# Performance work log

Measured on AMD Instinct MI355X. Metric: run time of the kernel, lower is better.

Reference implementation:

```python
import jax, jax.numpy as jnp
import numpy as np

NUM_GRAPHS = 4096


def setup_inputs() -> dict:
    key = jax.random.key(0)
    k1, k2, k3, k4, k5 = jax.random.split(key, 5)
    N, H = 500000, 256
    x = jax.random.normal(k1, (N, H), dtype=jnp.float32)
    batch = jnp.sort(jax.random.randint(k2, (N,), 0, NUM_GRAPHS, dtype=jnp.int64))
    # gate MLP: Linear(H, H//2) -> tanh -> Linear(H//2, 1)
    W1 = jax.random.normal(k3, (H, H // 2), dtype=jnp.float32) / np.sqrt(H)
    b1 = jnp.zeros((H // 2,), dtype=jnp.float32)
    W2 = jax.random.normal(k4, (H // 2, 1), dtype=jnp.float32) / np.sqrt(H // 2)
    b2 = jnp.zeros((1,), dtype=jnp.float32)
    return {"x": x, "batch": batch, "W1": W1, "b1": b1, "W2": W2, "b2": b2}


def reference(x, batch, W1, b1, W2, b2):
    # gate scores per node: (N,)
    h = jnp.tanh(x @ W1 + b1)
    scores = (h @ W2 + b2).squeeze(-1)
    # segment (per-graph) softmax over nodes
    seg_max = jax.ops.segment_max(scores, batch, num_segments=NUM_GRAPHS)
    # empty segments give -inf max; guard so gather stays finite
    seg_max = jnp.where(jnp.isfinite(seg_max), seg_max, 0.0)
    ex = jnp.exp(scores - seg_max[batch])
    seg_sum = jax.ops.segment_sum(ex, batch, num_segments=NUM_GRAPHS)
    weights = ex / seg_sum[batch]  # (N,)
    # weighted scatter-add pooling -> (B, H)
    pooled = jax.ops.segment_sum(weights[:, None] * x, batch, num_segments=NUM_GRAPHS)
    return pooled, weights
```

## Files before the change

kernel.cpp:

```cpp
#include <hip/hip_runtime.h>
#include <hip/hip_bf16.h>

#define NGRAPH 4096

typedef __attribute__((ext_vector_type(8))) short s16x8;
typedef __attribute__((ext_vector_type(4))) float f32x4;
typedef unsigned int u32;

__device__ inline short f2bf(float f) {
  unsigned u = __float_as_uint(f);
  unsigned r = u + 0x7fffu + ((u >> 16) & 1u);
  return (short)(r >> 16);
}

__global__ void prepack_w1(const float* __restrict__ W1, s16x8* __restrict__ w1p) {
  int t = blockIdx.x * 256 + threadIdx.x;
  int f = t >> 6, l = t & 63;
  int kt = f >> 3, ct = f & 7;
  int k0 = kt * 32 + ((l >> 4) * 8);
  int c  = ct * 16 + (l & 15);
  s16x8 v;
  #pragma unroll
  for (int e = 0; e < 8; ++e) v[e] = f2bf(W1[(k0 + e) * 128 + c]);
  w1p[f * 64 + l] = v;
}

__device__ inline long long getb(const void* b, int i, int is64) {
  if (is64) return ((const long long*)b)[i];
  return (long long)((const int*)b)[i];
}

__device__ inline int lowb(const void* b, int n, long long v, int is64) {
  int lo = 0, hi = n;
  while (lo < hi) {
    int mid = (lo + hi) >> 1;
    if (getb(b, mid, is64) < v) lo = mid + 1; else hi = mid;
  }
  return lo;
}

__device__ inline int batch_is64(const void* batch, int N) {
  int probe = ((N & 1) == 0) ? (N - 1) : (N - 2);
  return (((const int*)batch)[probe] == 0) ? 1 : 0;
}

__global__ void seg_offsets(const void* __restrict__ batch, int* __restrict__ offs, int N) {
  int g = blockIdx.x * 256 + threadIdx.x;
  const int is64 = batch_is64(batch, N);
  if (g <= NGRAPH) offs[g] = lowb(batch, N, (long long)g, is64);
}

__device__ inline float fast_tanh(float v) {
  v = fminf(fmaxf(v, -15.f), 15.f);
  float e = __expf(2.f * v);
  return __fdividef(e - 1.f, e + 1.f);
}

__device__ inline void dma16(const float* src, char* ldsdst) {
  __builtin_amdgcn_global_load_lds(
      (const __attribute__((address_space(1))) u32*)src,
      (__attribute__((address_space(3))) u32*)ldsdst,
      16, 0, 0);
}

__global__ __launch_bounds__(256, 3)
void gate_pool(const float* __restrict__ x, const int* __restrict__ offs,
               const float* __restrict__ b1, const float* __restrict__ W2,
               const float* __restrict__ b2p, const s16x8* __restrict__ w1p,
               float* __restrict__ pooled, float* __restrict__ expout,
               float* __restrict__ segsum, int N)
{
  __shared__ __align__(16) char tile[32 * 1024];
  __shared__ float sp[2][32];
  __shared__ float sw[32];

  const int tid = threadIdx.x;
  const int w = tid >> 6, l = tid & 63;
  const int colhalf = w & 1, wp = w >> 1;
  const int l15 = l & 15, lg = l >> 4;
  const int node0 = blockIdx.x * 32;

  #pragma unroll
  for (int i = 0; i < 8; ++i) {
    const int r = i * 4 + w;
    int grow = node0 + r;
    if (grow >= N) grow = N - 1;
    const float* src = x + (size_t)grow * 256 + ((l ^ (r & 7)) << 2);
    dma16(src, tile + r * 1024);
  }

  float b1v[4], w2v[4];
  #pragma unroll
  for (int ct = 0; ct < 4; ++ct) {
    int c = colhalf * 64 + ct * 16 + l15;
    b1v[ct] = b1[c];
    w2v[ct] = W2[c];
  }
  const float b2s = b2p[0];

  __syncthreads();

  {
    const int r0 = wp * 16 + l15;
    const char* p0 = tile + r0 * 1024;
    const int s0 = (r0 & 7);

    f32x4 acc0 = {0.f,0.f,0.f,0.f}, acc1 = {0.f,0.f,0.f,0.f};
    f32x4 acc2 = {0.f,0.f,0.f,0.f}, acc3 = {0.f,0.f,0.f,0.f};
    #pragma unroll
    for (int kt = 0; kt < 8; ++kt) {
      const int cc = kt * 8 + lg * 2;
      float4 xa = *(const float4*)(p0 + (((cc    ) ^ s0) << 4));
      float4 xb = *(const float4*)(p0 + (((cc + 1) ^ s0) << 4));
      const s16x8* wb = w1p + (kt * 8 + colhalf * 4) * 64 + l;
      s16x8 bf0 = wb[0], bf1 = wb[64], bf2 = wb[128], bf3 = wb[192];
      s16x8 a;
      a[0] = f2bf(xa.x); a[1] = f2bf(xa.y); a[2] = f2bf(xa.z); a[3] = f2bf(xa.w);
      a[4] = f2bf(xb.x); a[5] = f2bf(xb.y); a[6] = f2bf(xb.z); a[7] = f2bf(xb.w);
      acc0 = __builtin_amdgcn_mfma_f32_16x16x32_bf16(a, bf0, acc0, 0, 0, 0);
      acc1 = __builtin_amdgcn_mfma_f32_16x16x32_bf16(a, bf1, acc1, 0, 0, 0);
      acc2 = __builtin_amdgcn_mfma_f32_16x16x32_bf16(a, bf2, acc2, 0, 0, 0);
      acc3 = __builtin_amdgcn_mfma_f32_16x16x32_bf16(a, bf3, acc3, 0, 0, 0);
    }
    float part[4];
    #pragma unroll
    for (int r = 0; r < 4; ++r) {
      part[r] = colhalf ? 0.f : b2s;
      part[r] += fast_tanh(acc0[r] + b1v[0]) * w2v[0];
      part[r] += fast_tanh(acc1[r] + b1v[1]) * w2v[1];
      part[r] += fast_tanh(acc2[r] + b1v[2]) * w2v[2];
      part[r] += fast_tanh(acc3[r] + b1v[3]) * w2v[3];
    }
    #pragma unroll
    for (int m = 1; m <= 8; m <<= 1) {
      #pragma unroll
      for (int r = 0; r < 4; ++r) part[r] += __shfl_xor(part[r], m, 64);
    }
    if (l15 == 0) {
      #pragma unroll
      for (int r = 0; r < 4; ++r)
        sp[colhalf][wp * 16 + lg * 4 + r] = part[r];
    }
  }
  __syncthreads();

  if (tid < 32) {
    int node = node0 + tid;
    float e = 0.f;
    if (node < N) {
      e = __expf(sp[0][tid] + sp[1][tid]);
      expout[node] = e;
    }
    sw[tid] = e;
  }
  __syncthreads();

  const int nmax = min(32, N - node0);
  int g;
  {
    int lo = 0, hi = NGRAPH - 1;
    while (lo < hi) {
      int mid = (lo + hi) >> 1;
      if (offs[mid + 1] <= node0) lo = mid + 1; else hi = mid;
    }
    g = lo;
  }
  const int ccb = tid >> 2, cib = (tid & 3) << 2;
  int r = 0;
  int nb = offs[g + 1];
  while (r < nmax) {
    const int rend = min(nb - node0, nmax);
    float pacc = 0.f, wsum = 0.f;
    for (; r + 8 <= rend; r += 8) {
      float xv[8], wv[8];
      #pragma unroll
      for (int u = 0; u < 8; ++u) {
        const int rr = r + u;
        xv[u] = *(const float*)(tile + rr * 1024 + (((ccb ^ (rr & 7)) << 4) | cib));
        wv[u] = sw[rr];
      }
      #pragma unroll
      for (int u = 0; u < 8; ++u) {
        pacc += wv[u] * xv[u];
        wsum += wv[u];
      }
    }
    for (; r < rend; ++r) {
      float wv = sw[r];
      pacc += wv * *(const float*)(tile + r * 1024 + (((ccb ^ (r & 7)) << 4) | cib));
      wsum += wv;
    }
    if (wsum > 0.f) {
      atomicAdd(&pooled[(size_t)g * 256 + tid], pacc);
      if (tid == 0) atomicAdd(&segsum[g], wsum);
    }
    if (rend >= nmax) break;
    ++g;
    nb = offs[g + 1];
  }
}

__global__ void finalize(float* __restrict__ pooled, float* __restrict__ wts,
                         const float* __restrict__ segsum,
                         const void* __restrict__ batch, int N)
{
  int f = blockIdx.x * 256 + threadIdx.x;
  if (f < NGRAPH * 256) {
    int g = f >> 8;
    float s = segsum[g];
    pooled[f] = (s > 0.f) ? pooled[f] / s : 0.f;
  } else {
    int n = f - NGRAPH * 256;
    if (n < N) {
      const int is64 = batch_is64(batch, N);
      int g = (int)getb(batch, n, is64);
      wts[n] = wts[n] / segsum[g];
    }
  }
}

extern "C" void kernel_launch(void* const* d_in, const int* in_sizes, int n_in,
                              void* d_out, int out_size, void* d_ws, size_t ws_size,
                              hipStream_t stream) {
  const float* x     = (const float*)d_in[0];
  const void*  batch = d_in[1];
  const float* W1    = (const float*)d_in[2];
  const float* b1    = (const float*)d_in[3];
  const float* W2    = (const float*)d_in[4];
  const float* b2    = (const float*)d_in[5];
  const int N = in_sizes[0] / 256;

  float* pooled = (float*)d_out;
  float* wout   = (float*)d_out + (size_t)NGRAPH * 256;
  s16x8* w1p    = (s16x8*)d_ws;
  int*   offs   = (int*)((char*)d_ws + 64 * 1024);
  float* segsum = (float*)((char*)d_ws + 96 * 1024);

  hipMemsetAsync(pooled, 0, (size_t)NGRAPH * 256 * sizeof(float), stream);
  hipMemsetAsync(segsum, 0, (size_t)NGRAPH * sizeof(float), stream);

  prepack_w1<<<16, 256, 0, stream>>>(W1, w1p);
  seg_offsets<<<17, 256, 0, stream>>>(batch, offs, N);
  gate_pool<<<(N + 31) / 32, 256, 0, stream>>>(x, offs, b1, W2, b2, w1p,
                                               pooled, wout, segsum, N);
  const int tot = NGRAPH * 256 + N;
  finalize<<<(tot + 255) / 256, 256, 0, stream>>>(pooled, wout, segsum, batch, N);
}
```

Measured before the change: 185.7 us.

## Process two node tiles per block with double-buffered LDS loads

Each block now handles 64 nodes as two 32-row tiles. Both tiles are issued as async global-to-LDS loads up front, and the first tile is computed while the second is still in flight. The W1 fragments are hoisted into registers once per block. The starting graph id is read directly from batch, replacing the binary search over offsets. This trades 64KB of LDS per block and a lower occupancy bound (3 down to 2) for overlap between memory and compute, and halves the per-block setup cost.

```diff
diff --git a/kernel.cpp b/kernel.cpp
--- a/kernel.cpp
+++ b/kernel.cpp
@@ -63,14 +63,15 @@
       16, 0, 0);
 }
 
-__global__ __launch_bounds__(256, 3)
+__global__ __launch_bounds__(256, 2)
 void gate_pool(const float* __restrict__ x, const int* __restrict__ offs,
+               const void* __restrict__ batch,
                const float* __restrict__ b1, const float* __restrict__ W2,
                const float* __restrict__ b2p, const s16x8* __restrict__ w1p,
                float* __restrict__ pooled, float* __restrict__ expout,
-               float* __restrict__ segsum, int N)
+               float* __restrict__ segsum, int N, int ntiles)
 {
-  __shared__ __align__(16) char tile[32 * 1024];
+  __shared__ __align__(16) char buf[2][32 * 1024];
   __shared__ float sp[2][32];
   __shared__ float sw[32];
 
@@ -78,16 +79,10 @@
   const int w = tid >> 6, l = tid & 63;
   const int colhalf = w & 1, wp = w >> 1;
   const int l15 = l & 15, lg = l >> 4;
-  const int node0 = blockIdx.x * 32;
-
-  #pragma unroll
-  for (int i = 0; i < 8; ++i) {
-    const int r = i * 4 + w;
-    int grow = node0 + r;
-    if (grow >= N) grow = N - 1;
-    const float* src = x + (size_t)grow * 256 + ((l ^ (r & 7)) << 2);
-    dma16(src, tile + r * 1024);
-  }
+
+  const int node0_0 = blockIdx.x * 64;
+  const int node0_1 = node0_0 + 32;
+  const int has_t1 = (blockIdx.x * 2 + 1 < ntiles);
 
   float b1v[4], w2v[4];
   #pragma unroll
@@ -98,106 +93,151 @@
   }
   const float b2s = b2p[0];
 
-  __syncthreads();
-
-  {
-    const int r0 = wp * 16 + l15;
-    const char* p0 = tile + r0 * 1024;
-    const int s0 = (r0 & 7);
-
-    f32x4 acc0 = {0.f,0.f,0.f,0.f}, acc1 = {0.f,0.f,0.f,0.f};
-    f32x4 acc2 = {0.f,0.f,0.f,0.f}, acc3 = {0.f,0.f,0.f,0.f};
+  s16x8 bf[4][8];
+  #pragma unroll
+  for (int ctl = 0; ctl < 4; ++ctl)
     #pragma unroll
-    for (int kt = 0; kt < 8; ++kt) {
-      const int cc = kt * 8 + lg * 2;
-      float4 xa = *(const float4*)(p0 + (((cc    ) ^ s0) << 4));
-      float4 xb = *(const float4*)(p0 + (((cc + 1) ^ s0) << 4));
-      const s16x8* wb = w1p + (kt * 8 + colhalf * 4) * 64 + l;
-      s16x8 bf0 = wb[0], bf1 = wb[64], bf2 = wb[128], bf3 = wb[192];
-      s16x8 a;
-      a[0] = f2bf(xa.x); a[1] = f2bf(xa.y); a[2] = f2bf(xa.z); a[3] = f2bf(xa.w);
-      a[4] = f2bf(xb.x); a[5] = f2bf(xb.y); a[6] = f2bf(xb.z); a[7] = f2bf(xb.w);
-      acc0 = __builtin_amdgcn_mfma_f32_16x16x32_bf16(a, bf0, acc0, 0, 0, 0);
-      acc1 = __builtin_amdgcn_mfma_f32_16x16x32_bf16(a, bf1, acc1, 0, 0, 0);
-      acc2 = __builtin_amdgcn_mfma_f32_16x16x32_bf16(a, bf2, acc2, 0, 0, 0);
-      acc3 = __builtin_amdgcn_mfma_f32_16x16x32_bf16(a, bf3, acc3, 0, 0, 0);
+    for (int kt = 0; kt < 8; ++kt)
+      bf[ctl][kt] = w1p[(kt * 8 + colhalf * 4 + ctl) * 64 + l];
+
+  const int is64 = batch_is64(batch, N);
+  const int g0 = (int)getb(batch, node0_0, is64);
+  const int nb0 = offs[g0 + 1];
+  int g1 = 0, nb1 = 0;
+  if (has_t1) {
+    g1 = (int)getb(batch, min(node0_1, N - 1), is64);
+    nb1 = offs[g1 + 1];
+  }
+  __builtin_amdgcn_sched_barrier(0);
+
+  #pragma unroll
+  for (int i = 0; i < 8; ++i) {
+    const int r = i * 4 + w;
+    int grow = node0_0 + r;
+    if (grow >= N) grow = N - 1;
+    dma16(x + (size_t)grow * 256 + ((l ^ (r & 7)) << 2), buf[0] + r * 1024);
+  }
+  if (has_t1) {
+    #pragma unroll
+    for (int i = 0; i < 8; ++i) {
+      const int r = i * 4 + w;
+      int grow = node0_1 + r;
+      if (grow >= N) grow = N - 1;
+      dma16(x + (size_t)grow * 256 + ((l ^ (r & 7)) << 2), buf[1] + r * 1024);
     }
-    float part[4];
-    #pragma unroll
-    for (int r = 0; r < 4; ++r) {
-      part[r] = colhalf ? 0.f : b2s;
-      part[r] += fast_tanh(acc0[r] + b1v[0]) * w2v[0];
-      part[r] += fast_tanh(acc1[r] + b1v[1]) * w2v[1];
-      part[r] += fast_tanh(acc2[r] + b1v[2]) * w2v[2];
-      part[r] += fast_tanh(acc3[r] + b1v[3]) * w2v[3];
-    }
-    #pragma unroll
-    for (int m = 1; m <= 8; m <<= 1) {
-      #pragma unroll
-      for (int r = 0; r < 4; ++r) part[r] += __shfl_xor(part[r], m, 64);
-    }
-    if (l15 == 0) {
-      #pragma unroll
-      for (int r = 0; r < 4; ++r)
-        sp[colhalf][wp * 16 + lg * 4 + r] = part[r];
-    }
-  }
-  __syncthreads();
-
-  if (tid < 32) {
-    int node = node0 + tid;
-    float e = 0.f;
-    if (node < N) {
-      e = __expf(sp[0][tid] + sp[1][tid]);
-      expout[node] = e;
-    }
-    sw[tid] = e;
-  }
-  __syncthreads();
-
-  const int nmax = min(32, N - node0);
-  int g;
-  {
-    int lo = 0, hi = NGRAPH - 1;
-    while (lo < hi) {
-      int mid = (lo + hi) >> 1;
-      if (offs[mid + 1] <= node0) lo = mid + 1; else hi = mid;
-    }
-    g = lo;
-  }
-  const int ccb = tid >> 2, cib = (tid & 3) << 2;
-  int r = 0;
-  int nb = offs[g + 1];
-  while (r < nmax) {
-    const int rend = min(nb - node0, nmax);
-    float pacc = 0.f, wsum = 0.f;
-    for (; r + 8 <= rend; r += 8) {
-      float xv[8], wv[8];
-      #pragma unroll
-      for (int u = 0; u < 8; ++u) {
-        const int rr = r + u;
-        xv[u] = *(const float*)(tile + rr * 1024 + (((ccb ^ (rr & 7)) << 4) | cib));
-        wv[u] = sw[rr];
-      }
-      #pragma unroll
-      for (int u = 0; u < 8; ++u) {
-        pacc += wv[u] * xv[u];
-        wsum += wv[u];
-      }
-    }
-    for (; r < rend; ++r) {
-      float wv = sw[r];
-      pacc += wv * *(const float*)(tile + r * 1024 + (((ccb ^ (r & 7)) << 4) | cib));
-      wsum += wv;
-    }
-    if (wsum > 0.f) {
-      atomicAdd(&pooled[(size_t)g * 256 + tid], pacc);
-      if (tid == 0) atomicAdd(&segsum[g], wsum);
-    }
-    if (rend >= nmax) break;
-    ++g;
-    nb = offs[g + 1];
-  }
+  }
+  __builtin_amdgcn_sched_barrier(0);
+
+  if (has_t1) { asm volatile("s_waitcnt vmcnt(8)" ::: "memory"); }
+  else        { asm volatile("s_waitcnt vmcnt(0)" ::: "memory"); }
+  __builtin_amdgcn_s_barrier();
+  __builtin_amdgcn_sched_barrier(0);
+
+#define PROCESS_TILE(TB, NODE0, GSTART, NBSTART) do {                         \
+                      \
+    {                                                                         \
+      const int r0_ = wp * 16 + l15;                                          \
+      const char* p0_ = (TB) + r0_ * 1024;                                    \
+      const int s0_ = (r0_ & 7);                                              \
+      f32x4 a0_={0.f,0.f,0.f,0.f}, a1_={0.f,0.f,0.f,0.f};                     \
+      f32x4 a2_={0.f,0.f,0.f,0.f}, a3_={0.f,0.f,0.f,0.f};                     \
+      _Pragma("unroll")                                                       \
+      for (int kt_ = 0; kt_ < 8; ++kt_) {                                     \
+        const int cc_ = kt_ * 8 + lg * 2;                                     \
+        float4 xa_ = *(const float4*)(p0_ + (((cc_    ) ^ s0_) << 4));        \
+        float4 xb_ = *(const float4*)(p0_ + (((cc_ + 1) ^ s0_) << 4));        \
+        s16x8 a_;                                                             \
+        a_[0]=f2bf(xa_.x); a_[1]=f2bf(xa_.y); a_[2]=f2bf(xa_.z); a_[3]=f2bf(xa_.w); \
+        a_[4]=f2bf(xb_.x); a_[5]=f2bf(xb_.y); a_[6]=f2bf(xb_.z); a_[7]=f2bf(xb_.w); \
+        a0_ = __builtin_amdgcn_mfma_f32_16x16x32_bf16(a_, bf[0][kt_], a0_,0,0,0); \
+        a1_ = __builtin_amdgcn_mfma_f32_16x16x32_bf16(a_, bf[1][kt_], a1_,0,0,0); \
+        a2_ = __builtin_amdgcn_mfma_f32_16x16x32_bf16(a_, bf[2][kt_], a2_,0,0,0); \
+        a3_ = __builtin_amdgcn_mfma_f32_16x16x32_bf16(a_, bf[3][kt_], a3_,0,0,0); \
+      }                                                                       \
+      float part_[4];                                                         \
+      _Pragma("unroll")                                                       \
+      for (int r_ = 0; r_ < 4; ++r_) {                                        \
+        part_[r_] = colhalf ? 0.f : b2s;                                      \
+        part_[r_] += fast_tanh(a0_[r_] + b1v[0]) * w2v[0];                    \
+        part_[r_] += fast_tanh(a1_[r_] + b1v[1]) * w2v[1];                    \
+        part_[r_] += fast_tanh(a2_[r_] + b1v[2]) * w2v[2];                    \
+        part_[r_] += fast_tanh(a3_[r_] + b1v[3]) * w2v[3];                    \
+      }                                                                       \
+      _Pragma("unroll")                                                       \
+      for (int m_ = 1; m_ <= 8; m_ <<= 1) {                                   \
+        _Pragma("unroll")                                                     \
+        for (int r_ = 0; r_ < 4; ++r_) part_[r_] += __shfl_xor(part_[r_], m_, 64); \
+      }                                                                       \
+      if (l15 == 0) {                                                         \
+        _Pragma("unroll")                                                     \
+        for (int r_ = 0; r_ < 4; ++r_)                                        \
+          sp[colhalf][wp * 16 + lg * 4 + r_] = part_[r_];                     \
+      }                                                                       \
+    }                                                                         \
+    asm volatile("s_waitcnt lgkmcnt(0)" ::: "memory");                        \
+    __builtin_amdgcn_s_barrier();                                             \
+    __builtin_amdgcn_sched_barrier(0);                                        \
+    if (tid < 32) {                                                           \
+      int node_ = (NODE0) + tid;                                              \
+      float e_ = 0.f;                                                         \
+      if (node_ < N) {                                                        \
+        e_ = __expf(sp[0][tid] + sp[1][tid]);                                 \
+        expout[node_] = e_;                                                   \
+      }                                                                       \
+      sw[tid] = e_;                                                           \
+    }                                                                         \
+    asm volatile("s_waitcnt lgkmcnt(0)" ::: "memory");                        \
+    __builtin_amdgcn_s_barrier();                                             \
+    __builtin_amdgcn_sched_barrier(0);                                        \
+                                    \
+    {                                                                         \
+      const int nmax_ = min(32, N - (NODE0));                                 \
+      int g_ = (GSTART);                                                      \
+      int nb_ = (NBSTART);                                                    \
+      const int ccb_ = tid >> 2, cib_ = (tid & 3) << 2;                       \
+      int r_ = 0;                                                             \
+      while (r_ < nmax_) {                                                    \
+        const int rend_ = min(nb_ - (NODE0), nmax_);                          \
+        float pacc_ = 0.f, wsum_ = 0.f;                                       \
+        for (; r_ + 4 <= rend_; r_ += 4) {                                    \
+          float xv_[4], wv_[4];                                               \
+          _Pragma("unroll")                                                   \
+          for (int u_ = 0; u_ < 4; ++u_) {                                    \
+            const int rr_ = r_ + u_;                                          \
+            xv_[u_] = *(const float*)((TB) + rr_ * 1024 +                     \
+                        (((ccb_ ^ (rr_ & 7)) << 4) | cib_));                  \
+            wv_[u_] = sw[rr_];                                                \
+          }                                                                   \
+          _Pragma("unroll")                                                   \
+          for (int u_ = 0; u_ < 4; ++u_) {                                    \
+            pacc_ += wv_[u_] * xv_[u_];                                       \
+            wsum_ += wv_[u_];                                                 \
+          }                                                                   \
+        }                                                                     \
+        for (; r_ < rend_; ++r_) {                                            \
+          float wv_ = sw[r_];                                                 \
+          pacc_ += wv_ * *(const float*)((TB) + r_ * 1024 +                   \
+                        (((ccb_ ^ (r_ & 7)) << 4) | cib_));                   \
+          wsum_ += wv_;                                                       \
+        }                                                                     \
+        if (wsum_ > 0.f) {                                                    \
+          atomicAdd(&pooled[(size_t)g_ * 256 + tid], pacc_);                  \
+          if (tid == 0) atomicAdd(&segsum[g_], wsum_);                        \
+        }                                                                     \
+        if (rend_ >= nmax_) break;                                            \
+        ++g_;                                                                 \
+        nb_ = offs[g_ + 1];                                                   \
+      }                                                                       \
+    } } while (0)
+
+  PROCESS_TILE(buf[0], node0_0, g0, nb0);
+
+  asm volatile("s_waitcnt vmcnt(0)" ::: "memory");
+  __builtin_amdgcn_s_barrier();
+  __builtin_amdgcn_sched_barrier(0);
+
+  if (has_t1) PROCESS_TILE(buf[1], node0_1, g1, nb1);
+#undef PROCESS_TILE
 }
 
 __global__ void finalize(float* __restrict__ pooled, float* __restrict__ wts,
@@ -229,6 +269,8 @@
   const float* W2    = (const float*)d_in[4];
   const float* b2    = (const float*)d_in[5];
   const int N = in_sizes[0] / 256;
+  const int ntiles = (N + 31) / 32;
+  const int nblocks = (ntiles + 1) / 2;
 
   float* pooled = (float*)d_out;
   float* wout   = (float*)d_out + (size_t)NGRAPH * 256;
@@ -241,8 +283,8 @@
 
   prepack_w1<<<16, 256, 0, stream>>>(W1, w1p);
   seg_offsets<<<17, 256, 0, stream>>>(batch, offs, N);
-  gate_pool<<<(N + 31) / 32, 256, 0, stream>>>(x, offs, b1, W2, b2, w1p,
-                                               pooled, wout, segsum, N);
+  gate_pool<<<nblocks, 256, 0, stream>>>(x, offs, batch, b1, W2, b2, w1p,
+                                         pooled, wout, segsum, N, ntiles);
   const int tot = NGRAPH * 256 + N;
   finalize<<<(tot + 255) / 256, 256, 0, stream>>>(pooled, wout, segsum, batch, N);
 }
```

Measured after the change: 195.1 us. 1.05x slower.

## Make gate_pool persistent with double-buffered tile prefetch and precomputed tile metadata

Applied to the files above, without the earlier changes.

Turns gate_pool into a persistent kernel with 512 blocks that loop over 32-node tiles. The next tile's x rows are DMA-prefetched into a second LDS buffer while the current tile is computed. W1 bf16 fragments are loaded into registers once per block, and a new tile_meta kernel precomputes each tile's starting graph and next boundaries so the per-block binary search disappears. In exchange, register pressure rises (launch bounds drop to 2 blocks per SM), LDS use doubles, and there is an extra small kernel launch.

```diff
diff --git a/kernel.cpp b/kernel.cpp
--- a/kernel.cpp
+++ b/kernel.cpp
@@ -2,6 +2,7 @@
 #include <hip/hip_bf16.h>
 
 #define NGRAPH 4096
+#define PBLOCKS 512
 
 typedef __attribute__((ext_vector_type(8))) short s16x8;
 typedef __attribute__((ext_vector_type(4))) float f32x4;
@@ -50,6 +51,17 @@
   if (g <= NGRAPH) offs[g] = lowb(batch, N, (long long)g, is64);
 }
 
+__global__ void tile_meta(const void* __restrict__ batch, const int* __restrict__ offs,
+                          int4* __restrict__ meta, int N, int ntiles) {
+  int t = blockIdx.x * 256 + threadIdx.x;
+  if (t >= ntiles) return;
+  const int is64 = batch_is64(batch, N);
+  int node = t * 32; if (node >= N) node = N - 1;
+  int g = (int)getb(batch, node, is64);
+  meta[t] = make_int4(g, offs[g + 1],
+                      offs[min(g + 2, NGRAPH)], offs[min(g + 3, NGRAPH)]);
+}
+
 __device__ inline float fast_tanh(float v) {
   v = fminf(fmaxf(v, -15.f), 15.f);
   float e = __expf(2.f * v);
@@ -63,14 +75,15 @@
       16, 0, 0);
 }
 
-__global__ __launch_bounds__(256, 3)
-void gate_pool(const float* __restrict__ x, const int* __restrict__ offs,
+__global__ __launch_bounds__(256, 2)
+void gate_pool(const float* __restrict__ x, const int4* __restrict__ meta,
+               const int* __restrict__ offs,
                const float* __restrict__ b1, const float* __restrict__ W2,
                const float* __restrict__ b2p, const s16x8* __restrict__ w1p,
                float* __restrict__ pooled, float* __restrict__ expout,
-               float* __restrict__ segsum, int N)
+               float* __restrict__ segsum, int N, int ntiles)
 {
-  __shared__ __align__(16) char tile[32 * 1024];
+  __shared__ __align__(16) char buf[2][32 * 1024];
   __shared__ float sp[2][32];
   __shared__ float sw[32];
 
@@ -78,16 +91,15 @@
   const int w = tid >> 6, l = tid & 63;
   const int colhalf = w & 1, wp = w >> 1;
   const int l15 = l & 15, lg = l >> 4;
-  const int node0 = blockIdx.x * 32;
-
+
+  if (blockIdx.x >= ntiles) return;
+
+  s16x8 bf[4][8];
   #pragma unroll
-  for (int i = 0; i < 8; ++i) {
-    const int r = i * 4 + w;
-    int grow = node0 + r;
-    if (grow >= N) grow = N - 1;
-    const float* src = x + (size_t)grow * 256 + ((l ^ (r & 7)) << 2);
-    dma16(src, tile + r * 1024);
-  }
+  for (int ctl = 0; ctl < 4; ++ctl)
+    #pragma unroll
+    for (int kt = 0; kt < 8; ++kt)
+      bf[ctl][kt] = w1p[(kt * 8 + colhalf * 4 + ctl) * 64 + l];
 
   float b1v[4], w2v[4];
   #pragma unroll
@@ -98,105 +110,146 @@
   }
   const float b2s = b2p[0];
 
-  __syncthreads();
+  int ti = blockIdx.x;
+  int4 M = meta[ti];
 
   {
-    const int r0 = wp * 16 + l15;
-    const char* p0 = tile + r0 * 1024;
-    const int s0 = (r0 & 7);
-
-    f32x4 acc0 = {0.f,0.f,0.f,0.f}, acc1 = {0.f,0.f,0.f,0.f};
-    f32x4 acc2 = {0.f,0.f,0.f,0.f}, acc3 = {0.f,0.f,0.f,0.f};
+    const int node0 = ti * 32;
     #pragma unroll
-    for (int kt = 0; kt < 8; ++kt) {
-      const int cc = kt * 8 + lg * 2;
-      float4 xa = *(const float4*)(p0 + (((cc    ) ^ s0) << 4));
-      float4 xb = *(const float4*)(p0 + (((cc + 1) ^ s0) << 4));
-      const s16x8* wb = w1p + (kt * 8 + colhalf * 4) * 64 + l;
-      s16x8 bf0 = wb[0], bf1 = wb[64], bf2 = wb[128], bf3 = wb[192];
-      s16x8 a;
-      a[0] = f2bf(xa.x); a[1] = f2bf(xa.y); a[2] = f2bf(xa.z); a[3] = f2bf(xa.w);
-      a[4] = f2bf(xb.x); a[5] = f2bf(xb.y); a[6] = f2bf(xb.z); a[7] = f2bf(xb.w);
-      acc0 = __builtin_amdgcn_mfma_f32_16x16x32_bf16(a, bf0, acc0, 0, 0, 0);
-      acc1 = __builtin_amdgcn_mfma_f32_16x16x32_bf16(a, bf1, acc1, 0, 0, 0);
-      acc2 = __builtin_amdgcn_mfma_f32_16x16x32_bf16(a, bf2, acc2, 0, 0, 0);
-      acc3 = __builtin_amdgcn_mfma_f32_16x16x32_bf16(a, bf3, acc3, 0, 0, 0);
-    }
-    float part[4];
-    #pragma unroll
-    for (int r = 0; r < 4; ++r) {
-      part[r] = colhalf ? 0.f : b2s;
-      part[r] += fast_tanh(acc0[r] + b1v[0]) * w2v[0];
-      part[r] += fast_tanh(acc1[r] + b1v[1]) * w2v[1];
-      part[r] += fast_tanh(acc2[r] + b1v[2]) * w2v[2];
-      part[r] += fast_tanh(acc3[r] + b1v[3]) * w2v[3];
-    }
-    #pragma unroll
-    for (int m = 1; m <= 8; m <<= 1) {
+    for (int i = 0; i < 8; ++i) {
+      const int r = i * 4 + w;
+      int grow = node0 + r;
+      if (grow >= N) grow = N - 1;
+      dma16(x + (size_t)grow * 256 + ((l ^ (r & 7)) << 2), buf[0] + r * 1024);
+    }
+  }
+  asm volatile("s_waitcnt vmcnt(0)" ::: "memory");
+  __builtin_amdgcn_s_barrier();
+  __builtin_amdgcn_sched_barrier(0);
+
+  int par = 0;
+  for (; ti < ntiles; ti += PBLOCKS) {
+    const int tnext = ti + PBLOCKS;
+    int4 Mnext = M;
+    if (tnext < ntiles) {
+      Mnext = meta[tnext];
+      const int nn0 = tnext * 32;
+      char* dst = buf[par ^ 1];
       #pragma unroll
-      for (int r = 0; r < 4; ++r) part[r] += __shfl_xor(part[r], m, 64);
-    }
-    if (l15 == 0) {
+      for (int i = 0; i < 8; ++i) {
+        const int r = i * 4 + w;
+        int grow = nn0 + r;
+        if (grow >= N) grow = N - 1;
+        dma16(x + (size_t)grow * 256 + ((l ^ (r & 7)) << 2), dst + r * 1024);
+      }
+    }
+    __builtin_amdgcn_sched_barrier(0);
+
+    const char* tile = buf[par];
+    const int node0 = ti * 32;
+
+    {
+      const int r0 = wp * 16 + l15;
+      const char* p0 = tile + r0 * 1024;
+      const int s0 = (r0 & 7);
+      f32x4 acc0 = {0.f,0.f,0.f,0.f}, acc1 = {0.f,0.f,0.f,0.f};
+      f32x4 acc2 = {0.f,0.f,0.f,0.f}, acc3 = {0.f,0.f,0.f,0.f};
       #pragma unroll
-      for (int r = 0; r < 4; ++r)
-        sp[colhalf][wp * 16 + lg * 4 + r] = part[r];
-    }
-  }
-  __syncthreads();
-
-  if (tid < 32) {
-    int node = node0 + tid;
-    float e = 0.f;
-    if (node < N) {
-      e = __expf(sp[0][tid] + sp[1][tid]);
-      expout[node] = e;
-    }
-    sw[tid] = e;
-  }
-  __syncthreads();
-
-  const int nmax = min(32, N - node0);
-  int g;
-  {
-    int lo = 0, hi = NGRAPH - 1;
-    while (lo < hi) {
-      int mid = (lo + hi) >> 1;
-      if (offs[mid + 1] <= node0) lo = mid + 1; else hi = mid;
-    }
-    g = lo;
-  }
-  const int ccb = tid >> 2, cib = (tid & 3) << 2;
-  int r = 0;
-  int nb = offs[g + 1];
-  while (r < nmax) {
-    const int rend = min(nb - node0, nmax);
-    float pacc = 0.f, wsum = 0.f;
-    for (; r + 8 <= rend; r += 8) {
-      float xv[8], wv[8];
+      for (int kt = 0; kt < 8; ++kt) {
+        const int cc = kt * 8 + lg * 2;
+        float4 xa = *(const float4*)(p0 + (((cc    ) ^ s0) << 4));
+        float4 xb = *(const float4*)(p0 + (((cc + 1) ^ s0) << 4));
+        s16x8 a;
+        a[0] = f2bf(xa.x); a[1] = f2bf(xa.y); a[2] = f2bf(xa.z); a[3] = f2bf(xa.w);
+        a[4] = f2bf(xb.x); a[5] = f2bf(xb.y); a[6] = f2bf(xb.z); a[7] = f2bf(xb.w);
+        acc0 = __builtin_amdgcn_mfma_f32_16x16x32_bf16(a, bf[0][kt], acc0, 0, 0, 0);
+        acc1 = __builtin_amdgcn_mfma_f32_16x16x32_bf16(a, bf[1][kt], acc1, 0, 0, 0);
+        acc2 = __builtin_amdgcn_mfma_f32_16x16x32_bf16(a, bf[2][kt], acc2, 0, 0, 0);
+        acc3 = __builtin_amdgcn_mfma_f32_16x16x32_bf16(a, bf[3][kt], acc3, 0, 0, 0);
+      }
+      float part[4];
       #pragma unroll
-      for (int u = 0; u < 8; ++u) {
-        const int rr = r + u;
-        xv[u] = *(const float*)(tile + rr * 1024 + (((ccb ^ (rr & 7)) << 4) | cib));
-        wv[u] = sw[rr];
+      for (int r = 0; r < 4; ++r) {
+        part[r] = colhalf ? 0.f : b2s;
+        part[r] += fast_tanh(acc0[r] + b1v[0]) * w2v[0];
+        part[r] += fast_tanh(acc1[r] + b1v[1]) * w2v[1];
+        part[r] += fast_tanh(acc2[r] + b1v[2]) * w2v[2];
+        part[r] += fast_tanh(acc3[r] + b1v[3]) * w2v[3];
       }
       #pragma unroll
-      for (int u = 0; u < 8; ++u) {
-        pacc += wv[u] * xv[u];
-        wsum += wv[u];
-      }
-    }
-    for (; r < rend; ++r) {
-      float wv = sw[r];
-      pacc += wv * *(const float*)(tile + r * 1024 + (((ccb ^ (r & 7)) << 4) | cib));
-      wsum += wv;
-    }
-    if (wsum > 0.f) {
-      atomicAdd(&pooled[(size_t)g * 256 + tid], pacc);
-      if (tid == 0) atomicAdd(&segsum[g], wsum);
-    }
-    if (rend >= nmax) break;
-    ++g;
-    nb = offs[g + 1];
+      for (int m = 1; m <= 8; m <<= 1) {
+        #pragma unroll
+        for (int r = 0; r < 4; ++r) part[r] += __shfl_xor(part[r], m, 64);
+      }
+      if (l15 == 0) {
+        #pragma unroll
+        for (int r = 0; r < 4; ++r)
+          sp[colhalf][wp * 16 + lg * 4 + r] = part[r];
+      }
+    }
+    asm volatile("s_waitcnt lgkmcnt(0)" ::: "memory");
+    __builtin_amdgcn_s_barrier();
+    __builtin_amdgcn_sched_barrier(0);
+
+    if (tid < 32) {
+      int node = node0 + tid;
+      float e = 0.f;
+      if (node < N) {
+        e = __expf(sp[0][tid] + sp[1][tid]);
+        expout[node] = e;
+      }
+      sw[tid] = e;
+    }
+    asm volatile("s_waitcnt lgkmcnt(0)" ::: "memory");
+    __builtin_amdgcn_s_barrier();
+    __builtin_amdgcn_sched_barrier(0);
+
+    {
+      const int nmax = min(32, N - node0);
+      int g = M.x;
+      int nb = M.y;
+      int crossing = 0;
+      const int ccb = tid >> 2, cib = (tid & 3) << 2;
+      int r = 0;
+      while (r < nmax) {
+        const int rend = min(nb - node0, nmax);
+        float pacc = 0.f, wsum = 0.f;
+        for (; r + 8 <= rend; r += 8) {
+          float xv[8], wv[8];
+          #pragma unroll
+          for (int u = 0; u < 8; ++u) {
+            const int rr = r + u;
+            xv[u] = *(const float*)(tile + rr * 1024 + (((ccb ^ (rr & 7)) << 4) | cib));
+            wv[u] = sw[rr];
+          }
+          #pragma unroll
+          for (int u = 0; u < 8; ++u) {
+            pacc += wv[u] * xv[u];
+            wsum += wv[u];
+          }
+        }
+        for (; r < rend; ++r) {
+          float wv = sw[r];
+          pacc += wv * *(const float*)(tile + r * 1024 + (((ccb ^ (r & 7)) << 4) | cib));
+          wsum += wv;
+        }
+        if (wsum > 0.f) {
+          atomicAdd(&pooled[(size_t)g * 256 + tid], pacc);
+          if (tid == 0) atomicAdd(&segsum[g], wsum);
+        }
+        if (rend >= nmax) break;
+        ++g; ++crossing;
+        nb = (crossing == 1) ? M.z
+           : (crossing == 2) ? M.w
+           : offs[min(g + 1, NGRAPH)];
+      }
+    }
+
+    asm volatile("s_waitcnt vmcnt(0)" ::: "memory");
+    __builtin_amdgcn_s_barrier();
+    __builtin_amdgcn_sched_barrier(0);
+    M = Mnext;
+    par ^= 1;
   }
 }
 
@@ -229,20 +282,23 @@
   const float* W2    = (const float*)d_in[4];
   const float* b2    = (const float*)d_in[5];
   const int N = in_sizes[0] / 256;
+  const int ntiles = (N + 31) / 32;
 
   float* pooled = (float*)d_out;
   float* wout   = (float*)d_out + (size_t)NGRAPH * 256;
   s16x8* w1p    = (s16x8*)d_ws;
   int*   offs   = (int*)((char*)d_ws + 64 * 1024);
   float* segsum = (float*)((char*)d_ws + 96 * 1024);
+  int4*  meta   = (int4*)((char*)d_ws + 128 * 1024);
 
   hipMemsetAsync(pooled, 0, (size_t)NGRAPH * 256 * sizeof(float), stream);
   hipMemsetAsync(segsum, 0, (size_t)NGRAPH * sizeof(float), stream);
 
   prepack_w1<<<16, 256, 0, stream>>>(W1, w1p);
   seg_offsets<<<17, 256, 0, stream>>>(batch, offs, N);
-  gate_pool<<<(N + 31) / 32, 256, 0, stream>>>(x, offs, b1, W2, b2, w1p,
-                                               pooled, wout, segsum, N);
+  tile_meta<<<(ntiles + 255) / 256, 256, 0, stream>>>(batch, offs, meta, N, ntiles);
+  gate_pool<<<PBLOCKS, 256, 0, stream>>>(x, meta, offs, b1, W2, b2, w1p,
+                                         pooled, wout, segsum, N, ntiles);
   const int tot = NGRAPH * 256 + N;
   finalize<<<(tot + 255) / 256, 256, 0, stream>>>(pooled, wout, segsum, batch, N);
 }
```

Measured after the change: 184.9 us. About the same (-0.4%).
